# Performance work log

Measured on AMD Instinct MI355X. Metric: run time of the kernel, lower is better.

The kernel has to match this reference:

```python
import jax, jax.numpy as jnp
import numpy as np

TEMPERATURE = 10.0
EPS = 1e-12  # torch F.normalize eps


def setup_inputs() -> dict:
    key = jax.random.key(0)
    k1, k2 = jax.random.split(key)
    B, D = 8192, 1024
    text_embeddings = jax.random.normal(k1, (B, D), dtype=jnp.float32)
    image_embeddings = jax.random.normal(k2, (B, D), dtype=jnp.float32)
    bias = jnp.zeros((1,), dtype=jnp.float32)
    return {
        "text_embeddings": text_embeddings,
        "image_embeddings": image_embeddings,
        "bias": bias,
    }


def _normalize(x):
    # matches torch F.normalize(p=2, dim=1): x / max(||x||, eps)
    norm = jnp.linalg.norm(x, axis=-1, keepdims=True)
    return x / jnp.maximum(norm, EPS)


def reference(text_embeddings, image_embeddings, bias):
    B = text_embeddings.shape[0]
    img_n = _normalize(image_embeddings)   # [B, D]
    txt_n = _normalize(text_embeddings)    # [B, D]
    # similarity[i, j] = <img_i, txt_j>
    sim = jnp.einsum('id,jd->ij', img_n, txt_n)          # [B, B]
    logits = sim * (-TEMPERATURE) + bias[0]
    labels = 2.0 * jnp.eye(B, dtype=logits.dtype) - 1.0   # +1 diag, -1 off-diag
    # loss_ij = log(1/(1+exp(label*logit))) = -softplus(label*logit)
    total_loss = -jnp.sum(jax.nn.softplus(labels * logits))
    return -(total_loss / B)
```

## Files before the change

### kernel.cpp

```cpp
#include <hip/hip_runtime.h>
#include <stdint.h>
#include <stddef.h>

#define NROWS 8192
#define DIM   1024
#define RB    512
#define TEMP  10.0f

#define BM 128
#define BN 128

typedef __attribute__((ext_vector_type(4))) int i32x4;
typedef __attribute__((ext_vector_type(8))) int i32x8;
typedef __attribute__((ext_vector_type(16))) float floatx16;

__device__ __forceinline__ void load16_lds(const unsigned char* g, unsigned char* l) {
    __builtin_amdgcn_global_load_lds(
        (__attribute__((address_space(1))) void*)(g),
        (__attribute__((address_space(3))) void*)(l),
        16, 0, 0);
}

__device__ __forceinline__ unsigned fp4q(float x) {
    float a = fabsf(x);
    a = fminf(a, 6.0f);
    unsigned c = (unsigned)(a >= 0.25f) + (unsigned)(a >= 0.75f)
               + (unsigned)(a >= 1.25f) + (unsigned)(a >= 1.75f)
               + (unsigned)(a >= 2.5f)  + (unsigned)(a >= 3.5f)
               + (unsigned)(a >= 5.0f);
    return c | ((__float_as_uint(x) >> 28) & 8u);
}

__device__ __forceinline__ i32x8 op8u(i32x4 lo) {
    return __builtin_shufflevector(lo, lo, 0, 1, 2, 3, -1, -1, -1, -1);
}


__global__ __launch_bounds__(256) void normalize_kernel(
    const float* __restrict__ img, const float* __restrict__ txt,
    unsigned char* __restrict__ imgq, unsigned char* __restrict__ txtq,
    float* __restrict__ out)
{
    __shared__ __align__(16) unsigned short sc[4][256];
    const int t = threadIdx.x;
    const int lane = t & 63, wave = t >> 6;
    const int gw = blockIdx.x * 4 + wave;
    const float* src = (gw < NROWS) ? img + (size_t)gw * DIM
                                    : txt + (size_t)(gw - NROWS) * DIM;
    float4 v[4];
    float ss = 0.f;
#pragma unroll
    for (int c = 0; c < 4; c++) {
        v[c] = ((const float4*)src)[lane + 64 * c];
        ss += v[c].x * v[c].x + v[c].y * v[c].y + v[c].z * v[c].z + v[c].w * v[c].w;
    }
#pragma unroll
    for (int off = 32; off; off >>= 1) ss += __shfl_xor(ss, off);
    const float scale = 32.0f / fmaxf(sqrtf(ss), 1e-12f);
#pragma unroll
    for (int c = 0; c < 4; c++) {
        unsigned p = fp4q(v[c].x * scale)
                   | (fp4q(v[c].y * scale) << 4)
                   | (fp4q(v[c].z * scale) << 8)
                   | (fp4q(v[c].w * scale) << 12);
        sc[wave][c * 64 + lane] = (unsigned short)p;
    }
    __syncthreads();
    if (t < 128) {
        const int rr = t & 3, k = t >> 2;
        const int gr0 = blockIdx.x * 4;
        unsigned char* dq = (gr0 < NROWS) ? imgq : txtq;
        const int r = (gr0 < NROWS ? gr0 : gr0 - NROWS) + rr;
        const int4 d = *(const int4*)&sc[rr][k * 8];
        const int it = k >> 2, ks = (k >> 1) & 1, fh = k & 1;
        *(int4*)(dq + (size_t)it * 524288 + (size_t)((r >> 5) * 2048
                 + ks * 1024 + fh * 512 + (r & 31) * 16)) = d;
    }
    if (gw == 0 && lane == 0) out[0] = 0.f;
}

__global__ __launch_bounds__(512, 4) void simloss_kernel(
    const unsigned char* __restrict__ An,
    const unsigned char* __restrict__ Bn,
    const float* __restrict__ bias,
    float* __restrict__ out)
{
    __shared__ __align__(16) unsigned char As[8 * 8192];
    __shared__ float red[3][8];

    const int t = threadIdx.x;
    const int lane = t & 63;
    const int wave = t >> 6;

    const int bid = blockIdx.x;
    const int blockM = bid >> 3;
    const int n0 = bid & 7;

    {
        const unsigned char* gA = An + (size_t)blockM * 8192 + t * 16;
#pragma unroll
        for (int it = 0; it < 8; it++)
            load16_lds(gA + (size_t)it * 524288, As + it * 8192 + t * 16);
    }
    asm volatile("s_waitcnt vmcnt(0)" ::: "memory");
    __syncthreads();

    const int rgHalf = wave >> 1;
    const int nHalf = wave & 1;
    const int fr = lane & 31;
    const int fh = lane >> 5;
    const int vA0 = rgHalf * 2048 + lane * 16;

    const float bv = bias[0];
    const float c1 = -TEMP * 1.4426950408889634f / 1024.0f;
    const float c0 = bv * 1.4426950408889634f;

    const bool diagAny = (blockM & 7) == n0;
    const int jd = blockM >> 3;

    float accP = 0.f, accQ = 0.f, accD = 0.f;

    for (int j = 0; j < 8; ++j) {
        const int n = n0 + 8 * j;
        const unsigned char* gB = Bn
            + (size_t)((n * 4 + nHalf * 2) * 2048 + lane * 16);

        floatx16 acc[2];
        acc[0] = (floatx16)(0.f);
        acc[1] = (floatx16)(0.f);

        i32x4 aE[2], aO[2], bE[4], bO[4];
#pragma unroll
        for (int ks = 0; ks < 2; ks++)
            aE[ks] = *(const i32x4*)&As[vA0 + ks * 1024];
#pragma unroll
        for (int q = 0; q < 4; q++)
            bE[q] = *(const i32x4*)(gB + (q & 1) * 2048 + (q >> 1) * 1024);

#pragma unroll
        for (int pp = 0; pp < 4; ++pp) {
#pragma unroll
            for (int ks = 0; ks < 2; ks++)
                aO[ks] = *(const i32x4*)&As[vA0 + (2 * pp + 1) * 8192 + ks * 1024];
#pragma unroll
            for (int q = 0; q < 4; q++)
                bO[q] = *(const i32x4*)(gB + (size_t)(2 * pp + 1) * 524288
                                        + (q & 1) * 2048 + (q >> 1) * 1024);
#pragma unroll
            for (int ks = 0; ks < 2; ks++)
#pragma unroll
                for (int ni = 0; ni < 2; ni++)
                    acc[ni] = __builtin_amdgcn_mfma_scale_f32_32x32x64_f8f6f4(
                        op8u(aE[ks]), op8u(bE[ks * 2 + ni]), acc[ni],
                        4, 4,
                        0, 0x7f7f7f7f,
                        0, 0x7f7f7f7f);
            if (pp < 3) {
#pragma unroll
                for (int ks = 0; ks < 2; ks++)
                    aE[ks] = *(const i32x4*)&As[vA0 + (2 * pp + 2) * 8192 + ks * 1024];
#pragma unroll
                for (int q = 0; q < 4; q++)
                    bE[q] = *(const i32x4*)(gB + (size_t)(2 * pp + 2) * 524288
                                            + (q & 1) * 2048 + (q >> 1) * 1024);
            }
#pragma unroll
            for (int ks = 0; ks < 2; ks++)
#pragma unroll
                for (int ni = 0; ni < 2; ni++)
                    acc[ni] = __builtin_amdgcn_mfma_scale_f32_32x32x64_f8f6f4(
                        op8u(aO[ks]), op8u(bO[ks * 2 + ni]), acc[ni],
                        4, 4,
                        0, 0x7f7f7f7f,
                        0, 0x7f7f7f7f);
        }

#pragma unroll
        for (int ni = 0; ni < 2; ni++) {
#pragma unroll
            for (int g = 0; g < 2; g++) {
                float prod = 1.0f;
#pragma unroll
                for (int r8 = 0; r8 < 8; r8++) {
                    float sv = acc[ni][g * 8 + r8];
                    float w = fmaf(sv, c1, c0);
                    float aw = fabsf(w);
                    prod *= 1.0f + __builtin_amdgcn_exp2f(-aw);
                    accP = fmaf(0.5f, aw, accP);
                    accQ += sv;
                }
                accP += __builtin_amdgcn_logf(prod);
            }
        }
        if (diagAny && j == jd) {
            const int gi0 = blockM * BM + rgHalf * 32 + 4 * fh;
            const int gj0 = n * BN + nHalf * 64 + fr;
#pragma unroll
            for (int ni = 0; ni < 2; ni++)
#pragma unroll
                for (int reg = 0; reg < 16; reg++) {
                    int ig = gi0 + (reg & 3) + 8 * (reg >> 2);
                    int jg = gj0 + ni * 32;
                    if (ig == jg) accD += acc[ni][reg];
                }
        }
    }

#pragma unroll
    for (int off = 32; off; off >>= 1) {
        accP += __shfl_xor(accP, off);
        accQ += __shfl_xor(accQ, off);
        accD += __shfl_xor(accD, off);
    }
    if (lane == 0) {
        red[0][wave] = accP;
        red[1][wave] = accQ;
        red[2][wave] = accD;
    }
    __syncthreads();
    if (t == 0) {
        float P = 0.f, Q = 0.f, D = 0.f;
#pragma unroll
        for (int w = 0; w < 8; w++) {
            P += red[0][w];
            Q += red[1][w];
            D += red[2][w];
        }
        float contrib = fmaf(0.6931471805599453f, P,
                             fmaf(5.0f / 1024.0f, Q, (-TEMP / 1024.0f) * D));
        contrib += fmaf(-65536.0f, bv, diagAny ? 128.0f * bv : 0.f);
        atomicAdd(out, contrib * (1.0f / 8192.0f));
    }
}

extern "C" void kernel_launch(void* const* d_in, const int* in_sizes, int n_in,
                              void* d_out, int out_size, void* d_ws, size_t ws_size,
                              hipStream_t stream) {
    const float* txt = (const float*)d_in[0];
    const float* img = (const float*)d_in[1];
    const float* bias = (const float*)d_in[2];
    float* out = (float*)d_out;

    unsigned char* imgq = (unsigned char*)d_ws;
    unsigned char* txtq = imgq + (size_t)NROWS * RB;

    normalize_kernel<<<dim3(2 * NROWS / 4), dim3(256), 0, stream>>>(
        img, txt, imgq, txtq, out);

    simloss_kernel<<<dim3((NROWS / BM) * 8), dim3(512), 0, stream>>>(
        imgq, txtq, bias, out);
}
```

Measured before the change: 143.0 us.

## Stage B tiles through double-buffered LDS with async global-to-LDS loads

Each wave used to read its B fragments straight from global memory, so the four row-group waves fetched the same B data separately. Now each 8 KB B k-slice is copied once per block into a two-slot LDS buffer with global_load_lds, prefetching the next slice while MFMAs run on the current one. The price is a block-wide barrier on every k-step, 64 per block, each covering only four MFMAs per wave. The final block reduction through shared memory is also replaced by one atomicAdd per wave.

```diff
diff --git a/kernel.cpp b/kernel.cpp
--- a/kernel.cpp
+++ b/kernel.cpp
@@ -86,7 +86,7 @@
     float* __restrict__ out)
 {
     __shared__ __align__(16) unsigned char As[8 * 8192];
-    __shared__ float red[3][8];
+    __shared__ __align__(16) unsigned char Bs[2][8192];
 
     const int t = threadIdx.x;
     const int lane = t & 63;
@@ -101,15 +101,15 @@
 #pragma unroll
         for (int it = 0; it < 8; it++)
             load16_lds(gA + (size_t)it * 524288, As + it * 8192 + t * 16);
-    }
-    asm volatile("s_waitcnt vmcnt(0)" ::: "memory");
-    __syncthreads();
+        load16_lds(Bn + (size_t)n0 * 8192 + t * 16, &Bs[0][t * 16]);
+    }
 
     const int rgHalf = wave >> 1;
     const int nHalf = wave & 1;
     const int fr = lane & 31;
     const int fh = lane >> 5;
     const int vA0 = rgHalf * 2048 + lane * 16;
+    const int vB0 = nHalf * 4096 + lane * 16;
 
     const float bv = bias[0];
     const float c1 = -TEMP * 1.4426950408889634f / 1024.0f;
@@ -121,55 +121,34 @@
     float accP = 0.f, accQ = 0.f, accD = 0.f;
 
     for (int j = 0; j < 8; ++j) {
-        const int n = n0 + 8 * j;
-        const unsigned char* gB = Bn
-            + (size_t)((n * 4 + nHalf * 2) * 2048 + lane * 16);
-
         floatx16 acc[2];
         acc[0] = (floatx16)(0.f);
         acc[1] = (floatx16)(0.f);
 
-        i32x4 aE[2], aO[2], bE[4], bO[4];
-#pragma unroll
-        for (int ks = 0; ks < 2; ks++)
-            aE[ks] = *(const i32x4*)&As[vA0 + ks * 1024];
-#pragma unroll
-        for (int q = 0; q < 4; q++)
-            bE[q] = *(const i32x4*)(gB + (q & 1) * 2048 + (q >> 1) * 1024);
-
-#pragma unroll
-        for (int pp = 0; pp < 4; ++pp) {
+        for (int it = 0; it < 8; ++it) {
+            const int s = j * 8 + it;
+            __syncthreads();
+            if (s < 63) {
+                const int s1 = s + 1;
+                const int n1 = n0 + 8 * (s1 >> 3);
+                load16_lds(Bn + (size_t)(s1 & 7) * 524288 + (size_t)n1 * 8192
+                               + t * 16,
+                           &Bs[s1 & 1][t * 16]);
+            }
+            i32x4 a[2], b[4];
 #pragma unroll
             for (int ks = 0; ks < 2; ks++)
-                aO[ks] = *(const i32x4*)&As[vA0 + (2 * pp + 1) * 8192 + ks * 1024];
+                a[ks] = *(const i32x4*)&As[vA0 + it * 8192 + ks * 1024];
 #pragma unroll
             for (int q = 0; q < 4; q++)
-                bO[q] = *(const i32x4*)(gB + (size_t)(2 * pp + 1) * 524288
-                                        + (q & 1) * 2048 + (q >> 1) * 1024);
+                b[q] = *(const i32x4*)&Bs[s & 1][vB0 + (q >> 1) * 2048
+                                               + (q & 1) * 1024];
 #pragma unroll
             for (int ks = 0; ks < 2; ks++)
 #pragma unroll
                 for (int ni = 0; ni < 2; ni++)
                     acc[ni] = __builtin_amdgcn_mfma_scale_f32_32x32x64_f8f6f4(
-                        op8u(aE[ks]), op8u(bE[ks * 2 + ni]), acc[ni],
-                        4, 4,
-                        0, 0x7f7f7f7f,
-                        0, 0x7f7f7f7f);
-            if (pp < 3) {
-#pragma unroll
-                for (int ks = 0; ks < 2; ks++)
-                    aE[ks] = *(const i32x4*)&As[vA0 + (2 * pp + 2) * 8192 + ks * 1024];
-#pragma unroll
-                for (int q = 0; q < 4; q++)
-                    bE[q] = *(const i32x4*)(gB + (size_t)(2 * pp + 2) * 524288
-                                            + (q & 1) * 2048 + (q >> 1) * 1024);
-            }
-#pragma unroll
-            for (int ks = 0; ks < 2; ks++)
-#pragma unroll
-                for (int ni = 0; ni < 2; ni++)
-                    acc[ni] = __builtin_amdgcn_mfma_scale_f32_32x32x64_f8f6f4(
-                        op8u(aO[ks]), op8u(bO[ks * 2 + ni]), acc[ni],
+                        op8u(a[ks]), op8u(b[ni * 2 + ks]), acc[ni],
                         4, 4,
                         0, 0x7f7f7f7f,
                         0, 0x7f7f7f7f);
@@ -194,7 +173,7 @@
         }
         if (diagAny && j == jd) {
             const int gi0 = blockM * BM + rgHalf * 32 + 4 * fh;
-            const int gj0 = n * BN + nHalf * 64 + fr;
+            const int gj0 = blockM * BN + nHalf * 64 + fr;
 #pragma unroll
             for (int ni = 0; ni < 2; ni++)
 #pragma unroll
@@ -213,23 +192,12 @@
         accD += __shfl_xor(accD, off);
     }
     if (lane == 0) {
-        red[0][wave] = accP;
-        red[1][wave] = accQ;
-        red[2][wave] = accD;
-    }
-    __syncthreads();
-    if (t == 0) {
-        float P = 0.f, Q = 0.f, D = 0.f;
-#pragma unroll
-        for (int w = 0; w < 8; w++) {
-            P += red[0][w];
-            Q += red[1][w];
-            D += red[2][w];
-        }
-        float contrib = fmaf(0.6931471805599453f, P,
-                             fmaf(5.0f / 1024.0f, Q, (-TEMP / 1024.0f) * D));
-        contrib += fmaf(-65536.0f, bv, diagAny ? 128.0f * bv : 0.f);
-        atomicAdd(out, contrib * (1.0f / 8192.0f));
+        float wcon = fmaf(0.6931471805599453f, accP,
+                          fmaf(5.0f / 1024.0f, accQ,
+                               (-TEMP / 1024.0f) * accD));
+        if (wave == 0)
+            wcon += fmaf(-65536.0f, bv, diagAny ? 128.0f * bv : 0.f);
+        atomicAdd(out, wcon * (1.0f / 8192.0f));
     }
 }
 
```

Measured after the change: 185.6 us. 29.8% more time.
